# Kernel tuning notes

Measured on AMD Instinct MI355X. Metric: run time of the kernel, lower is better.

Reference implementation:

```python
import jax, jax.numpy as jnp
import numpy as np

N = 50000      # nodes
E = 800000     # edges (before self-loops)
IN = 256       # input_dim
HID = 72       # hidden_dim
HEADS = 4
NEG_SLOPE = 0.2  # PyG GATConv default leaky-relu slope


def setup_inputs() -> dict:
    key = jax.random.key(0)
    ks = jax.random.split(key, 16)
    rn = lambda k, shape: jax.random.normal(k, shape, jnp.float32) * 0.05
    return {
        "x": jax.random.normal(ks[0], (N, IN), jnp.float32),
        "edge_index": jax.random.randint(ks[1], (2, E), 0, N),
        "W_in": rn(ks[2], (IN, HID)), "b_in": jnp.zeros((HID,), jnp.float32),
        "W1": rn(ks[3], (HID, HEADS * HID)),
        "a_src1": rn(ks[4], (HEADS, HID)), "a_dst1": rn(ks[5], (HEADS, HID)),
        "b1": jnp.zeros((HEADS * HID,), jnp.float32),
        "W2": rn(ks[6], (HEADS * HID, HID)),
        "a_src2": rn(ks[7], (1, HID)), "a_dst2": rn(ks[8], (1, HID)),
        "b2": jnp.zeros((HID,), jnp.float32),
        "W3": rn(ks[9], (HID, HID)),
        "a_src3": rn(ks[10], (1, HID)), "a_dst3": rn(ks[11], (1, HID)),
        "b3": jnp.zeros((HID,), jnp.float32),
        "Ws1": rn(ks[12], (HID, 32)), "bs1": jnp.zeros((32,), jnp.float32),
        "Ws2": rn(ks[13], (32, 1)), "bs2": jnp.zeros((1,), jnp.float32),
    }


def gat_conv(x, src, dst, W, a_src, a_dst, bias, concat):
    # PyG GATConv (eval mode): per-head linear, leaky-relu attention logits,
    # segment softmax over incoming edges per destination, scatter-aggregate.
    H, C = a_src.shape
    h = (x @ W).reshape(-1, H, C)                      # [N, H, C]
    logit_s = jnp.einsum('nhc,hc->nh', h, a_src)       # [N, H]
    logit_d = jnp.einsum('nhc,hc->nh', h, a_dst)       # [N, H]
    e = jax.nn.leaky_relu(logit_s[src] + logit_d[dst], NEG_SLOPE)   # [Et, H]
    emax = jax.ops.segment_max(e, dst, num_segments=N)
    emax = jnp.where(jnp.isfinite(emax), emax, 0.0)
    p = jnp.exp(e - emax[dst])
    denom = jax.ops.segment_sum(p, dst, num_segments=N)
    alpha = p / jnp.maximum(denom[dst], 1e-16)         # [Et, H]
    out = jax.ops.segment_sum(h[src] * alpha[:, :, None], dst, num_segments=N)
    out = out.reshape(-1, H * C) if concat else out.mean(axis=1)
    return out + bias


def reference(x, edge_index, W_in, b_in,
              W1, a_src1, a_dst1, b1,
              W2, a_src2, a_dst2, b2,
              W3, a_src3, a_dst3, b3,
              Ws1, bs1, Ws2, bs2):
    loops = jnp.arange(N)                              # PyG add_self_loops=True
    src = jnp.concatenate([edge_index[0], loops])
    dst = jnp.concatenate([edge_index[1], loops])
    x0 = x @ W_in + b_in                               # [N, HID]
    h = jax.nn.elu(gat_conv(x0, src, dst, W1, a_src1, a_dst1, b1, True))
    h = jax.nn.elu(gat_conv(h, src, dst, W2, a_src2, a_dst2, b2, False))
    h = jax.nn.elu(gat_conv(h, src, dst, W3, a_src3, a_dst3, b3, False))
    h = h + x0
    score = jax.nn.relu(h @ Ws1 + bs1) @ Ws2 + bs2     # dropout = identity (eval)
    return score.squeeze(-1)                           # [N]
```

## Files before the change

### kernel.cpp

```cpp
#include <hip/hip_runtime.h>
#include <hip/hip_fp16.h>
#include <cmath>

#define NN 50000
#define EE 800000
#define ET (EE + NN)
#define IN_DIM 256
#define HID 72
#define CAP 96

typedef __attribute__((ext_vector_type(8))) short s8v;
typedef __attribute__((ext_vector_type(4))) short s4v;
typedef __attribute__((ext_vector_type(8))) __fp16 h8v;
typedef __attribute__((ext_vector_type(4))) float f4v;
typedef __attribute__((ext_vector_type(2))) float f2v;

__device__ __forceinline__ ushort f2bf(float x) {
    uint u = __float_as_uint(x);
    return (ushort)((u + 0x7fffu + ((u >> 16) & 1u)) >> 16);
}
__device__ __forceinline__ float bf2f(ushort h) {
    return __uint_as_float(((uint)h) << 16);
}
__device__ __forceinline__ void split4(const float4& v, s4v& h, s4v& l) {
    ushort h0 = f2bf(v.x), h1 = f2bf(v.y), h2 = f2bf(v.z), h3 = f2bf(v.w);
    h = (s4v){(short)h0, (short)h1, (short)h2, (short)h3};
    l = (s4v){(short)f2bf(v.x - bf2f(h0)), (short)f2bf(v.y - bf2f(h1)),
              (short)f2bf(v.z - bf2f(h2)), (short)f2bf(v.w - bf2f(h3))};
}
__device__ __forceinline__ f4v mfma16(s8v a, s8v b, f4v c) {
    return __builtin_amdgcn_mfma_f32_16x16x32_bf16(a, b, c, 0, 0, 0);
}
__device__ __forceinline__ f4v mfma16h(h8v a, h8v b, f4v c) {
    return __builtin_amdgcn_mfma_f32_16x16x32_f16(a, b, c, 0, 0, 0);
}
__device__ __forceinline__ f2v unpack_h2(uint pv) {
    __half2 hv = __builtin_bit_cast(__half2, pv);
    return (f2v){__low2float(hv), __high2float(hv)};
}
__device__ __forceinline__ uint pack_h2(float a, float b) {
    __half2 hp = __floats2half2_rn(a, b);
    return __builtin_bit_cast(uint, hp);
}
__device__ __forceinline__ f2v fma2(float w, f2v c, f2v a) {
    return __builtin_elementwise_fma((f2v){w, w}, c, a);
}

__device__ __forceinline__ void wsplit_one(const float* W, int ldw, int K,
        int idx, short* outH, short* outL) {
    int h = idx / (72 * K);
    int rem = idx - h * 72 * K;
    int n = rem / K, k = rem - n * K;
    float v = W[(size_t)k * ldw + h * 72 + n];
    ushort hi = f2bf(v);
    outH[idx] = (short)hi;
    outL[idx] = (short)f2bf(v - bf2f(hi));
}
__device__ __forceinline__ void wsplit_fp16(const float* W, int ldw, int K,
        int idx, ushort* outH, ushort* outL) {
    int h = idx / (72 * K);
    int rem = idx - h * 72 * K;
    int n = rem / K, k = rem - n * K;
    float v = W[(size_t)k * ldw + h * 72 + n];
    __half hi = __float2half_rn(v);
    float lo = (v - __half2float(hi)) * 2048.f;
    outH[idx] = __half_as_ushort(hi);
    outL[idx] = __half_as_ushort(__float2half_rn(lo));
}

#define PR0 18432
#define PR1 (PR0 + 20736)
#define PR2 (PR1 + 20736)
#define PR3 (PR2 + 5184)
#define PR4 (PR3 + 288)
#define PRTOT (PR4 + NN)

__global__ __launch_bounds__(256) void prep_kernel(
        const float* __restrict__ W_in, const float* __restrict__ W1,
        const float* __restrict__ W2, const float* __restrict__ W3,
        const float* __restrict__ a_src, const float* __restrict__ a_dst,
        short* __restrict__ BtInH, short* __restrict__ BtInL,
        ushort* __restrict__ Bt1H, ushort* __restrict__ Bt1L,
        ushort* __restrict__ Bt2H, ushort* __restrict__ Bt2L,
        short* __restrict__ Bt3H, short* __restrict__ Bt3L,
        float* __restrict__ wsrc, float* __restrict__ wdst,
        int* __restrict__ deg, ushort* __restrict__ ell) {
    int gid = blockIdx.x * 256 + threadIdx.x;
    if (gid < PR0) {
        wsplit_one(W_in, 72, 256, gid, BtInH, BtInL);
    } else if (gid < PR1) {
        wsplit_fp16(W1, 288, 72, gid - PR0, Bt1H, Bt1L);
    } else if (gid < PR2) {
        wsplit_fp16(W2, 72, 288, gid - PR1, Bt2H, Bt2L);
    } else if (gid < PR3) {
        wsplit_one(W3, 72, 72, gid - PR2, Bt3H, Bt3L);
    } else if (gid < PR4) {
        int j = gid - PR3;
        int h = j / HID, k = j % HID;
        const float* wrow = W1 + (size_t)k * (4 * HID) + h * HID;
        const float* as = a_src + h * HID;
        const float* ad = a_dst + h * HID;
        float s = 0.f, d = 0.f;
        for (int c = 0; c < HID; ++c) {
            float w = wrow[c];
            s = fmaf(w, as[c], s);
            d = fmaf(w, ad[c], d);
        }
        wsrc[j] = s;
        wdst[j] = d;
    } else if (gid < PRTOT) {
        int i = gid - PR4;
        deg[i] = 1;
        ell[(size_t)i * CAP] = (ushort)i;
    }
}

template <int NLOGIT, bool ELU_EPI, bool BATCHED, bool PACKOUT, bool APACK, bool ADJ>
__global__ __launch_bounds__(256) void gemm_mfma(
        const void* __restrict__ Ain, const short* __restrict__ BtH,
        const short* __restrict__ BtL, const float* __restrict__ bias,
        float* __restrict__ C, uint* __restrict__ Cp, int ldp,
        const float* __restrict__ lvs, const float* __restrict__ lvd,
        float* __restrict__ ls, float* __restrict__ ld,
        int M, int K, int lda, int Nfull,
        const int* __restrict__ eiw, int* __restrict__ degw,
        ushort* __restrict__ ellw, int gemmBlocks) {
    __shared__ __align__(16) short AhS[64 * 40], AlS[64 * 40];
    __shared__ __align__(16) short BhS[80 * 40], BlS[80 * 40];

    int tid = threadIdx.x;

    if (ADJ && (int)blockIdx.x >= gemmBlocks) {
        int t = (blockIdx.x - gemmBlocks) * 256 + tid;
        int i0 = t * 4;
        if (i0 < EE) {
            int4 s4 = *(const int4*)(eiw + i0);
            int4 d4 = *(const int4*)(eiw + EE + i0);
            int ss[4] = {s4.x, s4.y, s4.z, s4.w};
            int dd[4] = {d4.x, d4.y, d4.z, d4.w};
            #pragma unroll
            for (int u = 0; u < 4; ++u) {
                int pos = atomicAdd(&degw[dd[u]], 1);
                if (pos < CAP) ellw[(size_t)dd[u] * CAP + pos] = (ushort)ss[u];
            }
        }
        return;
    }

    int row0 = blockIdx.x * 64;
    int hh = BATCHED ? blockIdx.y : 0;
    int aoff = BATCHED ? hh * (APACK ? 36 : 72) : 0;
    int coff = BATCHED ? hh * 72 : 0;
    const short* bhg = BtH + (size_t)hh * 72 * K;
    const short* blg = BtL + (size_t)hh * 72 * K;

    for (int i = tid; i < 8 * 40; i += 256) {
        BhS[72 * 40 + i] = 0;
        BlS[72 * 40 + i] = 0;
    }

    int w = tid >> 6;
    int lane = tid & 63;
    int q = lane >> 4, l16 = lane & 15;

    f4v acc[5];
    #pragma unroll
    for (int f = 0; f < 5; ++f) acc[f] = (f4v)0.f;

    int ar = tid >> 2;
    int aseg = tid & 3;
    bool arok = (row0 + ar) < M;
    const float* aptrf = nullptr;
    const uint*  aptru = nullptr;
    if constexpr (APACK) {
        aptru = (const uint*)Ain + (size_t)(row0 + ar) * lda + aoff;
    } else {
        aptrf = (const float*)Ain + (size_t)(row0 + ar) * lda + aoff;
    }
    int bn0 = tid >> 2, bq0 = tid & 3;
    int bn1 = (tid + 256) >> 2;

    float4 va, vb;
    s8v bh0, bl0, bh1, bl1;
    auto gload = [&](int k0) {
        va = (float4){0, 0, 0, 0};
        vb = (float4){0, 0, 0, 0};
        int ka = k0 + aseg * 8;
        if constexpr (APACK) {
            if (arok && ka < K) {
                uint4 u = *(const uint4*)(aptru + (ka >> 1));
                f2v p0 = unpack_h2(u.x), p1 = unpack_h2(u.y);
                f2v p2 = unpack_h2(u.z), p3 = unpack_h2(u.w);
                va = (float4){p0.x, p0.y, p1.x, p1.y};
                vb = (float4){p2.x, p2.y, p3.x, p3.y};
            }
        } else {
            if (arok && ka < K)     va = *(const float4*)(aptrf + ka);
            if (arok && ka + 4 < K) vb = *(const float4*)(aptrf + ka + 4);
        }
        bh0 = (s8v)0; bl0 = (s8v)0;
        int kb = k0 + bq0 * 8;
        if (kb < K) {
            bh0 = *(const s8v*)(bhg + (size_t)bn0 * K + kb);
            bl0 = *(const s8v*)(blg + (size_t)bn0 * K + kb);
        }
        bh1 = (s8v)0; bl1 = (s8v)0;
        if (tid < 32 && kb < K) {
            bh1 = *(const s8v*)(bhg + (size_t)bn1 * K + kb);
            bl1 = *(const s8v*)(blg + (size_t)bn1 * K + kb);
        }
    };
    auto commit = [&]() {
        s4v h0, l0, h1, l1;
        split4(va, h0, l0);
        split4(vb, h1, l1);
        *(s4v*)&AhS[ar * 40 + aseg * 8]     = h0;
        *(s4v*)&AhS[ar * 40 + aseg * 8 + 4] = h1;
        *(s4v*)&AlS[ar * 40 + aseg * 8]     = l0;
        *(s4v*)&AlS[ar * 40 + aseg * 8 + 4] = l1;
        *(s8v*)&BhS[bn0 * 40 + bq0 * 8] = bh0;
        *(s8v*)&BlS[bn0 * 40 + bq0 * 8] = bl0;
        if (tid < 32) {
            *(s8v*)&BhS[bn1 * 40 + bq0 * 8] = bh1;
            *(s8v*)&BlS[bn1 * 40 + bq0 * 8] = bl1;
        }
    };

    int ntiles = (K + 31) / 32;
    gload(0);
    for (int t = 0; t < ntiles; ++t) {
        commit();
        __syncthreads();
        if (t + 1 < ntiles) gload((t + 1) * 32);
        s8v ah = *(const s8v*)&AhS[(w * 16 + l16) * 40 + q * 8];
        s8v al = *(const s8v*)&AlS[(w * 16 + l16) * 40 + q * 8];
        #pragma unroll
        for (int f = 0; f < 5; ++f) {
            s8v bh = *(const s8v*)&BhS[(f * 16 + l16) * 40 + q * 8];
            s8v bl = *(const s8v*)&BlS[(f * 16 + l16) * 40 + q * 8];
            acc[f] = mfma16(ah, bh, acc[f]);
            acc[f] = mfma16(ah, bl, acc[f]);
            acc[f] = mfma16(al, bh, acc[f]);
        }
        __syncthreads();
    }

    float v[5][4];
    #pragma unroll
    for (int f = 0; f < 5; ++f) {
        int col = f * 16 + l16;
        bool cv = col < 72;
        #pragma unroll
        for (int r = 0; r < 4; ++r) {
            float t = acc[f][r];
            if (cv && bias) t += bias[coff + col];
            if (ELU_EPI) t = (t > 0.f) ? t : expm1f(t);
            v[f][r] = cv ? t : 0.f;
        }
    }
    if (NLOGIT > 0) {
        #pragma unroll
        for (int h2 = 0; h2 < NLOGIT; ++h2) {
            #pragma unroll
            for (int r = 0; r < 4; ++r) {
                float s = 0.f, d = 0.f;
                #pragma unroll
                for (int f = 0; f < 5; ++f) {
                    int col = f * 16 + l16;
                    float lw = (col < 72) ? lvs[h2 * 72 + col] : 0.f;
                    float dw = (col < 72) ? lvd[h2 * 72 + col] : 0.f;
                    s = fmaf(v[f][r], lw, s);
                    d = fmaf(v[f][r], dw, d);
                }
                s += __shfl_xor(s, 1); s += __shfl_xor(s, 2);
                s += __shfl_xor(s, 4); s += __shfl_xor(s, 8);
                d += __shfl_xor(d, 1); d += __shfl_xor(d, 2);
                d += __shfl_xor(d, 4); d += __shfl_xor(d, 8);
                int gr = row0 + w * 16 + q * 4 + r;
                if (l16 == 0 && gr < M) {
                    ls[gr * NLOGIT + h2] = s;
                    ld[gr * NLOGIT + h2] = d;
                }
            }
        }
    }
    if (PACKOUT) {
        #pragma unroll
        for (int f = 0; f < 5; ++f) {
            int col = f * 16 + l16;
            #pragma unroll
            for (int r = 0; r < 4; ++r) {
                float vo = __shfl_xor(v[f][r], 1);
                if ((l16 & 1) == 0 && col < 72) {
                    int gr = row0 + w * 16 + q * 4 + r;
                    if (gr < M) {
                        Cp[(size_t)gr * ldp + ((coff + col) >> 1)] =
                            pack_h2(v[f][r], vo);
                    }
                }
            }
        }
    }
    if (C != nullptr) {
        #pragma unroll
        for (int f = 0; f < 5; ++f) {
            int col = f * 16 + l16;
            if (col >= 72) continue;
            #pragma unroll
            for (int r = 0; r < 4; ++r) {
                int gr = row0 + w * 16 + q * 4 + r;
                if (gr < M) C[(size_t)gr * Nfull + coff + col] = v[f][r];
            }
        }
    }
}

__global__ __launch_bounds__(256) void gemm12(
        const uint* __restrict__ a1p,
        const ushort* __restrict__ B1H, const ushort* __restrict__ B1L,
        const float* __restrict__ b1,
        const ushort* __restrict__ B2H, const ushort* __restrict__ B2L,
        const float* __restrict__ lvs, const float* __restrict__ lvd,
        float* __restrict__ lso, float* __restrict__ ldo,
        uint* __restrict__ outp) {
    __shared__ __align__(16) uint hS[64][148];
    const float LSC = 1.f / 2048.f;
    int tid = threadIdx.x;
    int w = tid >> 6;
    int lane = tid & 63;
    int q = lane >> 4, l16 = lane & 15;
    int row0 = blockIdx.x * 64;
    int arow = w * 16 + l16;
    int gra = row0 + arow;
    bool aok = gra < NN;
    const uint* abase = a1p + (size_t)(aok ? gra : 0) * 144;

    #pragma unroll
    for (int h = 0; h < 4; ++h) {
        f4v accH[5], accL[5];
        #pragma unroll
        for (int f = 0; f < 5; ++f) { accH[f] = (f4v)0.f; accL[f] = (f4v)0.f; }
        #pragma unroll
        for (int t3 = 0; t3 < 3; ++t3) {
            int ks = t3 * 32 + q * 8;
            h8v ah = (h8v)0;
            if (aok && ks < 72) {
                uint4 u = *(const uint4*)(abase + h * 36 + (ks >> 1));
                ah = __builtin_bit_cast(h8v, u);
            }
            #pragma unroll
            for (int f = 0; f < 5; ++f) {
                int bn = f * 16 + l16;
                h8v bh = (h8v)0, bl = (h8v)0;
                if (bn < 72 && ks < 72) {
                    bh = *(const h8v*)(B1H + ((size_t)h * 72 + bn) * 72 + ks);
                    bl = *(const h8v*)(B1L + ((size_t)h * 72 + bn) * 72 + ks);
                }
                accH[f] = mfma16h(ah, bh, accH[f]);
                accL[f] = mfma16h(ah, bl, accL[f]);
            }
        }
        #pragma unroll
        for (int f = 0; f < 5; ++f) {
            int col = f * 16 + l16;
            bool cv = col < 72;
            #pragma unroll
            for (int r = 0; r < 4; ++r) {
                float t = fmaf(accL[f][r], LSC, accH[f][r]);
                if (cv) {
                    t += b1[h * 72 + col];
                    t = (t > 0.f) ? t : expm1f(t);
                }
                float ve = cv ? t : 0.f;
                float vo = __shfl_xor(ve, 1);
                if ((l16 & 1) == 0 && col < 72) {
                    hS[w * 16 + q * 4 + r][h * 36 + (col >> 1)] = pack_h2(ve, vo);
                }
            }
        }
    }

    f4v accH[5], accL[5];
    #pragma unroll
    for (int f = 0; f < 5; ++f) { accH[f] = (f4v)0.f; accL[f] = (f4v)0.f; }
    #pragma unroll
    for (int t = 0; t < 9; ++t) {
        int ks = t * 32 + q * 8;
        uint4 u = *(const uint4*)&hS[arow][ks >> 1];
        h8v ah = __builtin_bit_cast(h8v, u);
        #pragma unroll
        for (int f = 0; f < 5; ++f) {
            int bn = f * 16 + l16;
            h8v bh = (h8v)0, bl = (h8v)0;
            if (bn < 72) {
                bh = *(const h8v*)(B2H + (size_t)bn * 288 + ks);
                bl = *(const h8v*)(B2L + (size_t)bn * 288 + ks);
            }
            accH[f] = mfma16h(ah, bh, accH[f]);
            accL[f] = mfma16h(ah, bl, accL[f]);
        }
    }
    float v[5][4];
    #pragma unroll
    for (int f = 0; f < 5; ++f) {
        int col = f * 16 + l16;
        bool cv = col < 72;
        #pragma unroll
        for (int r = 0; r < 4; ++r)
            v[f][r] = cv ? fmaf(accL[f][r], LSC, accH[f][r]) : 0.f;
    }
    #pragma unroll
    for (int r = 0; r < 4; ++r) {
        float s = 0.f, d = 0.f;
        #pragma unroll
        for (int f = 0; f < 5; ++f) {
            int col = f * 16 + l16;
            float lw = (col < 72) ? lvs[col] : 0.f;
            float dw = (col < 72) ? lvd[col] : 0.f;
            s = fmaf(v[f][r], lw, s);
            d = fmaf(v[f][r], dw, d);
        }
        s += __shfl_xor(s, 1); s += __shfl_xor(s, 2);
        s += __shfl_xor(s, 4); s += __shfl_xor(s, 8);
        d += __shfl_xor(d, 1); d += __shfl_xor(d, 2);
        d += __shfl_xor(d, 4); d += __shfl_xor(d, 8);
        int gr = row0 + w * 16 + q * 4 + r;
        if (l16 == 0 && gr < NN) {
            lso[gr] = s;
            ldo[gr] = d;
        }
    }
    #pragma unroll
    for (int f = 0; f < 5; ++f) {
        int col = f * 16 + l16;
        #pragma unroll
        for (int r = 0; r < 4; ++r) {
            float vo = __shfl_xor(v[f][r], 1);
            if ((l16 & 1) == 0 && col < 72) {
                int gr = row0 + w * 16 + q * 4 + r;
                if (gr < NN) outp[(size_t)gr * 36 + (col >> 1)] = pack_h2(v[f][r], vo);
            }
        }
    }
}

template <int H, bool EPI, bool ADD_RES, bool POUT, bool SCORE>
__global__ __launch_bounds__(64) void agg_gather(
        const uint* __restrict__ featp,
        const float* __restrict__ ls, const float* __restrict__ ld,
        const int* __restrict__ degv, const ushort* __restrict__ ell,
        const float* __restrict__ bias, const float* __restrict__ res,
        float* __restrict__ out, uint* __restrict__ outp,
        const float* __restrict__ Ws1, const float* __restrict__ bs1,
        const float* __restrict__ Ws2, const float* __restrict__ bs2,
        int n) {
    __shared__ float wsh[64 * H];
    __shared__ int ssh[64];
    __shared__ float srow[HID];
    int wid = blockIdx.x;
    int lane = threadIdx.x;
    int deg = min(degv[wid], CAP);
    const ushort* row = ell + (size_t)wid * CAP;

    float ldh[H];
    if (H == 4) {
        float4 t = ((const float4*)ld)[wid];
        ldh[0] = t.x; ldh[1] = t.y; ldh[2] = t.z; ldh[3] = t.w;
    } else {
        ldh[0] = ld[wid];
    }

    f2v acc2[H];
    #pragma unroll
    for (int h = 0; h < H; ++h) acc2[h] = (f2v)0.f;

    if (deg <= 64) {
        bool act = lane < deg;
        int s = row[act ? lane : 0];
        ssh[lane] = s;
        float e[H];
        float ev[H];
        if (H == 4) {
            float4 lv = ((const float4*)ls)[s];
            ev[0] = lv.x; ev[1] = lv.y; ev[2] = lv.z; ev[3] = lv.w;
        } else {
            ev[0] = ls[s];
        }
        #pragma unroll
        for (int h = 0; h < H; ++h) {
            float vv = ev[h] + ldh[h];
            vv = (vv > 0.f) ? vv : 0.2f * vv;
            e[h] = act ? vv : -__builtin_inff();
        }
        float wv[H];
        #pragma unroll
        for (int h = 0; h < H; ++h) {
            float mh = e[h];
            #pragma unroll
            for (int off = 32; off; off >>= 1) mh = fmaxf(mh, __shfl_xor(mh, off));
            float ph = act ? expf(e[h] - mh) : 0.f;
            float sh = ph;
            #pragma unroll
            for (int off = 32; off; off >>= 1) sh += __shfl_xor(sh, off);
            wv[h] = ph / fmaxf(sh, 1e-16f);
        }
        if (H == 4) {
            ((float4*)wsh)[lane] = (float4){wv[0], wv[1], wv[2], wv[3]};
        } else {
            wsh[lane] = wv[0];
        }
        __syncthreads();

        int nb = (deg + 7) & ~7;
        const uint* rowbase = featp + (lane < 36 ? lane : 0);
        for (int t = 0; t < nb; t += 8) {
            int si[8];
            #pragma unroll
            for (int u = 0; u < 8; ++u) si[u] = ssh[t + u];
            uint pv[8];
            #pragma unroll
            for (int u = 0; u < 8; ++u) pv[u] = rowbase[(size_t)si[u] * 36];
            #pragma unroll
            for (int u = 0; u < 8; ++u) {
                f2v c2 = unpack_h2(pv[u]);
                if constexpr (H == 4) {
                    float4 we = ((const float4*)wsh)[t + u];
                    acc2[0] = fma2(we.x, c2, acc2[0]);
                    acc2[1] = fma2(we.y, c2, acc2[1]);
                    acc2[2] = fma2(we.z, c2, acc2[2]);
                    acc2[3] = fma2(we.w, c2, acc2[3]);
                } else {
                    acc2[0] = fma2(wsh[t + u], c2, acc2[0]);
                }
            }
        }
    } else {
        float m[H];
        #pragma unroll
        for (int h = 0; h < H; ++h) m[h] = -__builtin_inff();
        for (int i = lane; i < deg; i += 64) {
            int s = row[i];
            float e[H];
            if (H == 4) {
                float4 lv = ((const float4*)ls)[s];
                e[0] = lv.x; e[1] = lv.y; e[2] = lv.z; e[3] = lv.w;
            } else {
                e[0] = ls[s];
            }
            #pragma unroll
            for (int h = 0; h < H; ++h) {
                float vv = e[h] + ldh[h];
                vv = (vv > 0.f) ? vv : 0.2f * vv;
                m[h] = fmaxf(m[h], vv);
            }
        }
        #pragma unroll
        for (int h = 0; h < H; ++h)
            #pragma unroll
            for (int off = 32; off; off >>= 1) m[h] = fmaxf(m[h], __shfl_xor(m[h], off));

        float ssum[H];
        #pragma unroll
        for (int h = 0; h < H; ++h) ssum[h] = 0.f;
        for (int i = lane; i < deg; i += 64) {
            int s = row[i];
            float e[H];
            if (H == 4) {
                float4 lv = ((const float4*)ls)[s];
                e[0] = lv.x; e[1] = lv.y; e[2] = lv.z; e[3] = lv.w;
            } else {
                e[0] = ls[s];
            }
            #pragma unroll
            for (int h = 0; h < H; ++h) {
                float vv = e[h] + ldh[h];
                vv = (vv > 0.f) ? vv : 0.2f * vv;
                ssum[h] += expf(vv - m[h]);
            }
        }
        #pragma unroll
        for (int h = 0; h < H; ++h)
            #pragma unroll
            for (int off = 32; off; off >>= 1) ssum[h] += __shfl_xor(ssum[h], off);
        float inv[H];
        #pragma unroll
        for (int h = 0; h < H; ++h) inv[h] = 1.f / fmaxf(ssum[h], 1e-16f);

        for (int base = 0; base < deg; base += 64) {
            int i = base + lane;
            int lim = min(64, deg - base);
            if (i < deg) {
                int s = row[i];
                ssh[lane] = s;
                float e[H];
                if (H == 4) {
                    float4 lv = ((const float4*)ls)[s];
                    e[0] = lv.x; e[1] = lv.y; e[2] = lv.z; e[3] = lv.w;
                } else {
                    e[0] = ls[s];
                }
                if (H == 4) {
                    float p0 = expf(((e[0] + ldh[0] > 0.f) ? e[0] + ldh[0] : 0.2f * (e[0] + ldh[0])) - m[0]) * inv[0];
                    float p1 = expf(((e[1] + ldh[1] > 0.f) ? e[1] + ldh[1] : 0.2f * (e[1] + ldh[1])) - m[1]) * inv[1];
                    float p2 = expf(((e[2] + ldh[2] > 0.f) ? e[2] + ldh[2] : 0.2f * (e[2] + ldh[2])) - m[2]) * inv[2];
                    float p3 = expf(((e[3] + ldh[3] > 0.f) ? e[3] + ldh[3] : 0.2f * (e[3] + ldh[3])) - m[3]) * inv[3];
                    ((float4*)wsh)[lane] = (float4){p0, p1, p2, p3};
                } else {
                    float vv = e[0] + ldh[0];
                    vv = (vv > 0.f) ? vv : 0.2f * vv;
                    wsh[lane] = expf(vv - m[0]) * inv[0];
                }
            }
            __syncthreads();
            for (int t = 0; t < lim; ++t) {
                uint pv = featp[(size_t)ssh[t] * 36 + (lane < 36 ? lane : 0)];
                f2v c2 = unpack_h2(pv);
                if constexpr (H == 4) {
                    float4 we = ((const float4*)wsh)[t];
                    acc2[0] = fma2(we.x, c2, acc2[0]);
                    acc2[1] = fma2(we.y, c2, acc2[1]);
                    acc2[2] = fma2(we.z, c2, acc2[2]);
                    acc2[3] = fma2(we.w, c2, acc2[3]);
                } else {
                    acc2[0] = fma2(wsh[t], c2, acc2[0]);
                }
            }
            __syncthreads();
        }
    }

    if (lane < 36) {
        #pragma unroll
        for (int h = 0; h < H; ++h) {
            float v0 = acc2[h].x, v1 = acc2[h].y;
            if (EPI) {
                v0 += bias[2 * lane];
                v1 += bias[2 * lane + 1];
                v0 = (v0 > 0.f) ? v0 : expm1f(v0);
                v1 = (v1 > 0.f) ? v1 : expm1f(v1);
                if (ADD_RES) {
                    float2 rr = *(const float2*)&res[(size_t)wid * HID + 2 * lane];
                    v0 += rr.x; v1 += rr.y;
                }
            }
            if (POUT) {
                outp[(size_t)wid * (H * 36) + h * 36 + lane] = pack_h2(v0, v1);
            } else if (SCORE) {
                srow[2 * lane] = v0;
                srow[2 * lane + 1] = v1;
            } else {
                *(float2*)&out[(size_t)wid * (H * HID) + h * HID + 2 * lane] =
                    (float2){v0, v1};
            }
        }
    }
    if (SCORE) {
        __syncthreads();
        if (lane < 32) {
            float acc = bs1[lane];
            #pragma unroll 8
            for (int c = 0; c < HID; ++c)
                acc = fmaf(srow[c], Ws1[c * 32 + lane], acc);
            float v = fmaxf(acc, 0.f) * Ws2[lane];
            #pragma unroll
            for (int off = 16; off; off >>= 1) v += __shfl_down(v, off, 32);
            if (lane == 0) out[wid] = v + bs2[0];
        }
    }
}

extern "C" void kernel_launch(void* const* d_in, const int* in_sizes, int n_in,
                              void* d_out, int out_size, void* d_ws, size_t ws_size,
                              hipStream_t stream) {
    const float* x      = (const float*)d_in[0];
    const int*   ei     = (const int*)  d_in[1];
    const float* W_in   = (const float*)d_in[2];
    const float* b_in   = (const float*)d_in[3];
    const float* W1     = (const float*)d_in[4];
    const float* a_src1 = (const float*)d_in[5];
    const float* a_dst1 = (const float*)d_in[6];
    const float* b1     = (const float*)d_in[7];
    const float* W2     = (const float*)d_in[8];
    const float* a_src2 = (const float*)d_in[9];
    const float* a_dst2 = (const float*)d_in[10];
    const float* b2     = (const float*)d_in[11];
    const float* W3     = (const float*)d_in[12];
    const float* a_src3 = (const float*)d_in[13];
    const float* a_dst3 = (const float*)d_in[14];
    const float* b3     = (const float*)d_in[15];
    const float* Ws1    = (const float*)d_in[16];
    const float* bs1    = (const float*)d_in[17];
    const float* Ws2    = (const float*)d_in[18];
    const float* bs2    = (const float*)d_in[19];
    float* out = (float*)d_out;

    float* ws    = (float*)d_ws;
    float* x0    = ws;
    float* ls    = x0 + (size_t)NN * HID;
    float* ld    = ls + (size_t)NN * 4;
    float* ls3   = ld + (size_t)NN * 4;
    float* ld3   = ls3 + NN;
    float* wsrc1 = ld3 + NN;
    float* wdst1 = wsrc1 + 288;
    int* deg     = (int*)(wdst1 + 288);
    ushort* ell  = (ushort*)(deg + NN);
    uintptr_t bp = ((uintptr_t)(ell + (size_t)NN * CAP) + 15) & ~(uintptr_t)15;
    short* BtInH = (short*)bp;
    short* BtInL = BtInH + 18432;
    ushort* Bt1H = (ushort*)(BtInL + 18432);
    ushort* Bt1L = Bt1H + 20736;
    ushort* Bt2H = Bt1L + 20736;
    ushort* Bt2L = Bt2H + 20736;
    short* Bt3H  = (short*)(Bt2L + 20736);
    short* Bt3L  = Bt3H + 5184;
    uint*  x0p   = (uint*)(Bt3L + 5184);
    uint*  a1p   = x0p + (size_t)NN * 36;
    uint*  hp2p  = a1p + (size_t)NN * 144;
    uint*  h2p   = hp2p + (size_t)NN * 36;
    uint*  hp3p  = h2p + (size_t)NN * 36;

    prep_kernel<<<(PRTOT + 255) / 256, 256, 0, stream>>>(
        W_in, W1, W2, W3, a_src1, a_dst1,
        BtInH, BtInL, Bt1H, Bt1L, Bt2H, Bt2L, Bt3H, Bt3L, wsrc1, wdst1,
        deg, ell);

    const int mblocks = (NN + 63) / 64;
    const int adjBlocks = (EE / 4 + 255) / 256;
    gemm_mfma<4, false, false, true, false, true>
        <<<dim3(mblocks + adjBlocks, 1), 256, 0, stream>>>(
        x, BtInH, BtInL, b_in, x0, x0p, 36, wsrc1, wdst1, ls, ld,
        NN, IN_DIM, IN_DIM, HID, ei, deg, ell, mblocks);
    agg_gather<4, false, false, true, false><<<NN, 64, 0, stream>>>(
        x0p, ls, ld, deg, ell, nullptr, nullptr, nullptr, a1p,
        nullptr, nullptr, nullptr, nullptr, NN);
    gemm12<<<mblocks, 256, 0, stream>>>(
        a1p, Bt1H, Bt1L, b1, Bt2H, Bt2L, a_src2, a_dst2, ls, ld, hp2p);
    agg_gather<1, true, false, true, false><<<NN, 64, 0, stream>>>(
        hp2p, ls, ld, deg, ell, b2, nullptr, nullptr, h2p,
        nullptr, nullptr, nullptr, nullptr, NN);
    gemm_mfma<1, false, false, true, true, false><<<dim3(mblocks, 1), 256, 0, stream>>>(
        h2p, Bt3H, Bt3L, nullptr, nullptr, hp3p, 36, a_src3, a_dst3, ls3, ld3,
        NN, HID, 36, 0, nullptr, nullptr, nullptr, 0);
    agg_gather<1, true, true, false, true><<<NN, 64, 0, stream>>>(
        hp3p, ls3, ld3, deg, ell, b3, x0, out, nullptr,
        Ws1, bs1, Ws2, bs2, NN);
}
```

Before: 391.2 us.

## Interleave per-head second GEMM in gemm12 to shrink LDS staging buffer

The second GEMM (288->72) is split into per-head chunks and accumulated right after each head's first-GEMM output is produced. The shared-memory staging buffer therefore holds only one head's 72 columns instead of all 288, cutting LDS from about 37KB to 10KB per block, which could raise occupancy. Each wave reads only its own rows, so no barrier is needed. The cost is extra live accumulator registers (a second set of 40 floats) held across the head loop, which may increase register pressure.

```diff
diff --git a/kernel.cpp b/kernel.cpp
--- a/kernel.cpp
+++ b/kernel.cpp
@@ -323,7 +323,7 @@
         const float* __restrict__ lvs, const float* __restrict__ lvd,
         float* __restrict__ lso, float* __restrict__ ldo,
         uint* __restrict__ outp) {
-    __shared__ __align__(16) uint hS[64][148];
+    __shared__ __align__(16) uint hS[64][40];
     const float LSC = 1.f / 2048.f;
     int tid = threadIdx.x;
     int w = tid >> 6;
@@ -335,11 +335,15 @@
     bool aok = gra < NN;
     const uint* abase = a1p + (size_t)(aok ? gra : 0) * 144;
 
+    f4v acc2H[5], acc2L[5];
+    #pragma unroll
+    for (int f = 0; f < 5; ++f) { acc2H[f] = (f4v)0.f; acc2L[f] = (f4v)0.f; }
+
     #pragma unroll
     for (int h = 0; h < 4; ++h) {
-        f4v accH[5], accL[5];
-        #pragma unroll
-        for (int f = 0; f < 5; ++f) { accH[f] = (f4v)0.f; accL[f] = (f4v)0.f; }
+        f4v aH[5], aL[5];
+        #pragma unroll
+        for (int f = 0; f < 5; ++f) { aH[f] = (f4v)0.f; aL[f] = (f4v)0.f; }
         #pragma unroll
         for (int t3 = 0; t3 < 3; ++t3) {
             int ks = t3 * 32 + q * 8;
@@ -356,8 +360,8 @@
                     bh = *(const h8v*)(B1H + ((size_t)h * 72 + bn) * 72 + ks);
                     bl = *(const h8v*)(B1L + ((size_t)h * 72 + bn) * 72 + ks);
                 }
-                accH[f] = mfma16h(ah, bh, accH[f]);
-                accL[f] = mfma16h(ah, bl, accL[f]);
+                aH[f] = mfma16h(ah, bh, aH[f]);
+                aL[f] = mfma16h(ah, bl, aL[f]);
             }
         }
         #pragma unroll
@@ -366,7 +370,7 @@
             bool cv = col < 72;
             #pragma unroll
             for (int r = 0; r < 4; ++r) {
-                float t = fmaf(accL[f][r], LSC, accH[f][r]);
+                float t = fmaf(aL[f][r], LSC, aH[f][r]);
                 if (cv) {
                     t += b1[h * 72 + col];
                     t = (t > 0.f) ? t : expm1f(t);
@@ -374,32 +378,33 @@
                 float ve = cv ? t : 0.f;
                 float vo = __shfl_xor(ve, 1);
                 if ((l16 & 1) == 0 && col < 72) {
-                    hS[w * 16 + q * 4 + r][h * 36 + (col >> 1)] = pack_h2(ve, vo);
-                }
-            }
-        }
-    }
-
-    f4v accH[5], accL[5];
-    #pragma unroll
-    for (int f = 0; f < 5; ++f) { accH[f] = (f4v)0.f; accL[f] = (f4v)0.f; }
-    #pragma unroll
-    for (int t = 0; t < 9; ++t) {
-        int ks = t * 32 + q * 8;
-        uint4 u = *(const uint4*)&hS[arow][ks >> 1];
-        h8v ah = __builtin_bit_cast(h8v, u);
-        #pragma unroll
-        for (int f = 0; f < 5; ++f) {
-            int bn = f * 16 + l16;
-            h8v bh = (h8v)0, bl = (h8v)0;
-            if (bn < 72) {
-                bh = *(const h8v*)(B2H + (size_t)bn * 288 + ks);
-                bl = *(const h8v*)(B2L + (size_t)bn * 288 + ks);
-            }
-            accH[f] = mfma16h(ah, bh, accH[f]);
-            accL[f] = mfma16h(ah, bl, accL[f]);
-        }
-    }
+                    hS[w * 16 + q * 4 + r][col >> 1] = pack_h2(ve, vo);
+                }
+            }
+        }
+
+        #pragma unroll
+        for (int t3 = 0; t3 < 3; ++t3) {
+            int ks = t3 * 32 + q * 8;
+            h8v ah2 = (h8v)0;
+            if (ks < 72) {
+                uint4 u = *(const uint4*)&hS[arow][ks >> 1];
+                ah2 = __builtin_bit_cast(h8v, u);
+            }
+            #pragma unroll
+            for (int f = 0; f < 5; ++f) {
+                int bn = f * 16 + l16;
+                h8v bh = (h8v)0, bl = (h8v)0;
+                if (bn < 72 && ks < 72) {
+                    bh = *(const h8v*)(B2H + (size_t)bn * 288 + h * 72 + ks);
+                    bl = *(const h8v*)(B2L + (size_t)bn * 288 + h * 72 + ks);
+                }
+                acc2H[f] = mfma16h(ah2, bh, acc2H[f]);
+                acc2L[f] = mfma16h(ah2, bl, acc2L[f]);
+            }
+        }
+    }
+
     float v[5][4];
     #pragma unroll
     for (int f = 0; f < 5; ++f) {
@@ -407,7 +412,7 @@
         bool cv = col < 72;
         #pragma unroll
         for (int r = 0; r < 4; ++r)
-            v[f][r] = cv ? fmaf(accL[f][r], LSC, accH[f][r]) : 0.f;
+            v[f][r] = cv ? fmaf(acc2L[f][r], LSC, acc2H[f][r]) : 0.f;
     }
     #pragma unroll
     for (int r = 0; r < 4; ++r) {
```

Result: no change. 387.7 us (-0.9%).
